# Performance work log

Measured on AMD Instinct MI355X. Metric: run time of the kernel, lower is better.

## Reference

```python
import jax, jax.numpy as jnp
import numpy as np

C = 256

def setup_inputs() -> dict:
    key = jax.random.key(0)
    ks = jax.random.split(key, 8)
    B, H, W = 4, 64, 64
    x = jax.random.normal(ks[0], (B, C, H, W), dtype=jnp.float32)
    # 1x1 conv weights ~ kaiming uniform; bias zero
    bound = np.sqrt(6.0 / C)
    Wq = jax.random.uniform(ks[1], (C, C), minval=-bound, maxval=bound, dtype=jnp.float32)
    Wk = jax.random.uniform(ks[2], (C, C), minval=-bound, maxval=bound, dtype=jnp.float32)
    Wv = jax.random.uniform(ks[3], (C, C), minval=-bound, maxval=bound, dtype=jnp.float32)
    bq = jnp.zeros((C,), jnp.float32)
    bk = jnp.zeros((C,), jnp.float32)
    bv = jnp.zeros((C,), jnp.float32)
    # gamma initialized to zero in torch; use small nonzero so output depends on attn path
    gamma = jnp.array([0.1], dtype=jnp.float32)
    return {"x": x, "Wq": Wq, "bq": bq, "Wk": Wk, "bk": bk, "Wv": Wv, "bv": bv, "gamma": gamma}


def reference(x, Wq, bq, Wk, bk, Wv, bv, gamma):
    B, Cc, H, W = x.shape
    N = H * W
    xf = x.reshape(B, Cc, N)  # [B,C,N]
    # 1x1 conv == per-pixel linear over channels: out[b,o,n] = sum_c W[o,c]*x[b,c,n] + b[o]
    q = jnp.einsum('oc,bcn->bon', Wq, xf) + bq[None, :, None]  # [B,C,N]
    k = jnp.einsum('oc,bcn->bon', Wk, xf) + bk[None, :, None]
    v = jnp.einsum('oc,bcn->bon', Wv, xf) + bv[None, :, None]
    # energy[b,i,j] = q[b,:,i] . k[b,:,j]  (no scaling, as in source)
    energy = jnp.einsum('bci,bcj->bij', q, k)  # [B,N,N]
    attention = jax.nn.softmax(energy, axis=-1)
    # out[b,c,i] = sum_j v[b,c,j] * attention[b,i,j]  (bmm(value, attn^T))
    out = jnp.einsum('bcj,bij->bci', v, attention)
    out = out.reshape(B, Cc, H, W)
    return gamma * out + x
```

## Files before the change

kernel.cpp:

```cpp
#include <hip/hip_runtime.h>
#include <hip/hip_bf16.h>
#include <cstdint>


#define C_DIM 256
#define N_DIM 4096
#define B_DIM 4

typedef _Float16 f16;
typedef f16 f16x8 __attribute__((ext_vector_type(8)));
typedef f16 f16x4 __attribute__((ext_vector_type(4)));
typedef float f32x4 __attribute__((ext_vector_type(4)));

__device__ __forceinline__ void dma16(const f16* g, f16* l) {
  __builtin_amdgcn_global_load_lds(
      (const __attribute__((address_space(1))) unsigned int*)g,
      (__attribute__((address_space(3))) unsigned int*)l, 16, 0, 0);
}

__global__ __launch_bounds__(256) void k_prep_xs(const float* __restrict__ x,
                                                 f16* __restrict__ xs) {
  __shared__ float tile[64][65];
  const int b = blockIdx.z, nb = blockIdx.x * 64, cb = blockIdx.y * 64;
  const float* xb = x + (size_t)b * C_DIM * N_DIM;
  for (int i = threadIdx.x; i < 64 * 64; i += 256) {
    int c = i >> 6, n = i & 63;
    tile[c][n] = xb[(size_t)(cb + c) * N_DIM + nb + n];
  }
  __syncthreads();
  f16* xsb = xs + (size_t)b * N_DIM * C_DIM;
  for (int i = threadIdx.x; i < 64 * 64; i += 256) {
    int n = i >> 6, c = i & 63;
    xsb[(size_t)(nb + n) * C_DIM + cb + c] = (f16)tile[c][n];
  }
}

__global__ __launch_bounds__(256) void k_cast_w(const float* __restrict__ Wq,
                                                const float* __restrict__ Wk,
                                                const float* __restrict__ Wv,
                                                f16* __restrict__ Wh) {
  int i = blockIdx.x * 256 + threadIdx.x;
  int sel = i >> 16, j = i & 65535;
  const float* s = (sel == 0) ? Wq : (sel == 1) ? Wk : Wv;
  Wh[i] = (f16)s[j];
}

__global__ __launch_bounds__(256) void k_proj(const f16* __restrict__ xs,
                                              const f16* __restrict__ Wh,
                                              const float* __restrict__ bq,
                                              const float* __restrict__ bk,
                                              const float* __restrict__ bv,
                                              f16* __restrict__ Qh,
                                              f16* __restrict__ Kh,
                                              f16* __restrict__ Vh) {
  const int z = blockIdx.y;
  const int w = threadIdx.x >> 6, lane = threadIdx.x & 63;
  const int quad = lane >> 4, li = lane & 15;
  const f16* W = Wh + (size_t)z * 65536;
  const float* bias = (z == 0) ? bq : (z == 1) ? bk : bv;

  if (z < 2) {
    f16* out = (z == 0) ? Qh : Kh;
    const int g0 = (blockIdx.x * 4 + w) * 16;
    f16x8 a[8];
    const f16* arow = xs + (size_t)(g0 + li) * C_DIM + quad * 8;
#pragma unroll
    for (int kf = 0; kf < 8; kf++) a[kf] = *(const f16x8*)(arow + kf * 32);
    for (int ot = 0; ot < 16; ot++) {
      f32x4 acc = {0.f, 0.f, 0.f, 0.f};
      const f16* brow = W + (size_t)(ot * 16 + li) * C_DIM + quad * 8;
#pragma unroll
      for (int kf = 0; kf < 8; kf++) {
        f16x8 bf = *(const f16x8*)(brow + kf * 32);
        acc = __builtin_amdgcn_mfma_f32_16x16x32_f16(a[kf], bf, acc, 0, 0, 0);
      }
      float bb = bias[ot * 16 + li];
      f16* orow = out + (size_t)g0 * C_DIM + ot * 16 + li;
#pragma unroll
      for (int r = 0; r < 4; r++)
        orow[(size_t)(quad * 4 + r) * C_DIM] = (f16)(acc[r] + bb);
    }
  } else {
    const int t = blockIdx.x * 4 + w;
    const int b = t >> 8, j0 = (t & 255) * 16;
    f16x8 bfr[8];
    const f16* brow = xs + (size_t)(b * N_DIM + j0 + li) * C_DIM + quad * 8;
#pragma unroll
    for (int kf = 0; kf < 8; kf++) bfr[kf] = *(const f16x8*)(brow + kf * 32);
    for (int ot = 0; ot < 16; ot++) {
      f32x4 acc = {0.f, 0.f, 0.f, 0.f};
      const f16* arow = W + (size_t)(ot * 16 + li) * C_DIM + quad * 8;
#pragma unroll
      for (int kf = 0; kf < 8; kf++) {
        f16x8 af = *(const f16x8*)(arow + kf * 32);
        acc = __builtin_amdgcn_mfma_f32_16x16x32_f16(af, bfr[kf], acc, 0, 0, 0);
      }
      f16* obase = Vh + ((size_t)(b * C_DIM + ot * 16 + quad * 4)) * N_DIM + j0 + li;
#pragma unroll
      for (int r = 0; r < 4; r++) {
        float bb = bias[ot * 16 + quad * 4 + r];
        obase[(size_t)r * N_DIM] = (f16)(acc[r] + bb);
      }
    }
  }
}

#define JT 64
#define NT (N_DIM / JT)
#define K0_OFF 0
#define K1_OFF 16384
#define V0_OFF 32768
#define V1_OFF 49152
#define P_OFF  65536
#define PSTR 72
#define SMEM_F16 70144

__global__ __launch_bounds__(256, 1) void k_attn(const f16* __restrict__ Qh,
                                                 const f16* __restrict__ Kh,
                                                 const f16* __restrict__ Vh,
                                                 const float* __restrict__ x,
                                                 const float* __restrict__ gamma_p,
                                                 float* __restrict__ out) {
  __shared__ __align__(16) f16 smem[SMEM_F16];
  const int b = blockIdx.y;
  const int tid = threadIdx.x;
  const int w = tid >> 6, lane = tid & 63;
  const int quad = lane >> 4, li = lane & 15;
  const int lw = li & 7;
  const int ibase = blockIdx.x * 64 + w * 16;

  int ksl[8];
#pragma unroll
  for (int kf = 0; kf < 8; kf++) ksl[kf] = ((kf * 4 + quad) ^ lw) << 3;
  const int vsl0 = (quad ^ lw) << 3;

  f16x8 qf[8];
  {
    const f16* qrow = Qh + (size_t)(b * N_DIM + ibase + li) * C_DIM + quad * 8;
#pragma unroll
    for (int kf = 0; kf < 8; kf++) qf[kf] = *(const f16x8*)(qrow + kf * 32);
  }
  const f16* Kb = Kh + (size_t)b * N_DIM * C_DIM;
  const f16* Vb = Vh + (size_t)b * C_DIM * N_DIM;
  f16* Pw = smem + P_OFF + w * 16 * PSTR;

  const float LOG2E = 1.4426950408889634f;
  float m = -3.0e38f, l = 0.0f;
  f32x4 acc[16];
#pragma unroll
  for (int ct = 0; ct < 16; ct++) acc[ct] = (f32x4){0.f, 0.f, 0.f, 0.f};

  {
    const f16* kg = Kb;
    const f16* vg = Vb;
#pragma unroll
    for (int it = 0; it < 8; it++) {
      int p = w * 8 + it;
      int krsw = (2 * it + (lane >> 5)) & 7;
      dma16(kg + (size_t)(2 * p + (lane >> 5)) * C_DIM + (((lane & 31) ^ krsw) * 8),
            smem + K0_OFF + p * 512);
      dma16(vg + (size_t)(p * 8 + (lane >> 3)) * N_DIM + (((lane & 7) ^ (lane >> 3)) * 8),
            smem + V0_OFF + p * 512);
    }
  }
  __syncthreads();

  for (int t = 0; t < NT; t++) {
    const f16* Kc = smem + ((t & 1) ? K1_OFF : K0_OFF);
    const f16* Vc = smem + ((t & 1) ? V1_OFF : V0_OFF);

    if (t + 1 < NT) {
      f16* Kn = smem + ((t & 1) ? K0_OFF : K1_OFF);
      f16* Vn = smem + ((t & 1) ? V0_OFF : V1_OFF);
      const int jt = (t + 1) * JT;
      const f16* kg = Kb + (size_t)jt * C_DIM;
      const f16* vg = Vb + jt;
#pragma unroll
      for (int it = 0; it < 8; it++) {
        int p = w * 8 + it;
        int krsw = (2 * it + (lane >> 5)) & 7;
        dma16(kg + (size_t)(2 * p + (lane >> 5)) * C_DIM + (((lane & 31) ^ krsw) * 8),
              Kn + p * 512);
        dma16(vg + (size_t)(p * 8 + (lane >> 3)) * N_DIM + (((lane & 7) ^ (lane >> 3)) * 8),
              Vn + p * 512);
      }
    }

    f32x4 s[4];
#pragma unroll
    for (int sub = 0; sub < 4; sub++) {
      f32x4 ss = {0.f, 0.f, 0.f, 0.f};
      const f16* krow = Kc + (sub * 16 + li) * 256;
#pragma unroll
      for (int kf = 0; kf < 8; kf++) {
        f16x8 kfr = *(const f16x8*)(krow + ksl[kf]);
        ss = __builtin_amdgcn_mfma_f32_16x16x32_f16(kfr, qf[kf], ss, 0, 0, 0);
      }
      s[sub] = ss;
    }

    float tm = -3.0e38f;
#pragma unroll
    for (int sub = 0; sub < 4; sub++)
      tm = fmaxf(tm, fmaxf(fmaxf(s[sub][0], s[sub][1]), fmaxf(s[sub][2], s[sub][3])));
    tm = fmaxf(tm, __shfl_xor(tm, 16));
    tm = fmaxf(tm, __shfl_xor(tm, 32));
    float nm = fmaxf(m, tm);
    float alpha = exp2f((m - nm) * LOG2E);
    m = nm;
    if (__any(alpha < 1.0f)) {
      l *= alpha;
#pragma unroll
      for (int ct = 0; ct < 16; ct++) {
        acc[ct][0] *= alpha; acc[ct][1] *= alpha;
        acc[ct][2] *= alpha; acc[ct][3] *= alpha;
      }
    }
#pragma unroll
    for (int sub = 0; sub < 4; sub++) {
      float p0 = exp2f((s[sub][0] - m) * LOG2E);
      float p1 = exp2f((s[sub][1] - m) * LOG2E);
      float p2 = exp2f((s[sub][2] - m) * LOG2E);
      float p3 = exp2f((s[sub][3] - m) * LOG2E);
      l += (p0 + p1) + (p2 + p3);
      *(f16x4*)(Pw + li * PSTR + sub * 16 + quad * 4) =
          (f16x4){(f16)p0, (f16)p1, (f16)p2, (f16)p3};
    }

    f16x8 pf0 = *(const f16x8*)(Pw + li * PSTR + quad * 8);
    f16x8 pf1 = *(const f16x8*)(Pw + li * PSTR + 32 + quad * 8);
#pragma unroll
    for (int ct = 0; ct < 16; ct++) {
      const f16* vrow = Vc + (ct * 16 + li) * 64;
      f16x8 v0 = *(const f16x8*)(vrow + vsl0);
      f16x8 v1 = *(const f16x8*)(vrow + (vsl0 ^ 32));
      acc[ct] = __builtin_amdgcn_mfma_f32_16x16x32_f16(v0, pf0, acc[ct], 0, 0, 0);
      acc[ct] = __builtin_amdgcn_mfma_f32_16x16x32_f16(v1, pf1, acc[ct], 0, 0, 0);
    }

    __syncthreads();
  }

  l += __shfl_xor(l, 16);
  l += __shfl_xor(l, 32);
  const float scale = gamma_p[0] / l;

  const float* xb = x + (size_t)b * C_DIM * N_DIM;
  float* ob = out + (size_t)b * C_DIM * N_DIM;
  const int icol = ibase + li;
#pragma unroll
  for (int ct = 0; ct < 16; ct++) {
#pragma unroll
    for (int r = 0; r < 4; r++) {
      size_t off = (size_t)(ct * 16 + quad * 4 + r) * N_DIM + icol;
      ob[off] = acc[ct][r] * scale + xb[off];
    }
  }
}

extern "C" void kernel_launch(void* const* d_in, const int* in_sizes, int n_in,
                              void* d_out, int out_size, void* d_ws, size_t ws_size,
                              hipStream_t stream) {
  const float* x     = (const float*)d_in[0];
  const float* Wq    = (const float*)d_in[1];
  const float* bq    = (const float*)d_in[2];
  const float* Wk    = (const float*)d_in[3];
  const float* bk    = (const float*)d_in[4];
  const float* Wv    = (const float*)d_in[5];
  const float* bv    = (const float*)d_in[6];
  const float* gamma = (const float*)d_in[7];
  float* out = (float*)d_out;

  char* ws = (char*)d_ws;
  f16* xs = (f16*)(ws);
  f16* Qh = (f16*)(ws + (size_t)8  * 1024 * 1024);
  f16* Kh = (f16*)(ws + (size_t)16 * 1024 * 1024);
  f16* Vh = (f16*)(ws + (size_t)24 * 1024 * 1024);
  f16* Wh = (f16*)(ws + (size_t)32 * 1024 * 1024);

  k_prep_xs<<<dim3(64, 4, 4), 256, 0, stream>>>(x, xs);
  k_cast_w<<<dim3(768), 256, 0, stream>>>(Wq, Wk, Wv, Wh);
  k_proj<<<dim3(256, 3), 256, 0, stream>>>(xs, Wh, bq, bk, bv, Qh, Kh, Vh);
  k_attn<<<dim3(64, 4), 256, 0, stream>>>(Qh, Kh, Vh, x, gamma, out);
}
```

Measured before the change: 294.6 us.

## Split each key tile across two wave groups with flash-style merge

The attention kernel doubles to 512 threads (8 waves). Each group of four waves processes half of every 64-key tile, keeping its own running max, sum and accumulators. At the end, the two halves are combined through shared memory with a log-sum-exp rescale. This is meant to double resident waves per CU, since there is only one block per CU, and so hide more MFMA and LDS latency. The cost is a cross-wave merge, extra shared-memory traffic, and twice as many waves holding large accumulator register sets.

Result: faster. 258.6 us (-12.2%).

```diff
diff --git a/kernel.cpp b/kernel.cpp
--- a/kernel.cpp
+++ b/kernel.cpp
@@ -112,10 +112,13 @@
 #define V0_OFF 32768
 #define V1_OFF 49152
 #define P_OFF  65536
-#define PSTR 72
-#define SMEM_F16 70144
-
-__global__ __launch_bounds__(256, 1) void k_attn(const f16* __restrict__ Qh,
+#define PSTR 40
+#define SMEM_F16 70656
+#define MRG_WSTR 4160
+#define MRG_CSTR 260
+#define ML_OFF   16640
+
+__global__ __launch_bounds__(512, 1) void k_attn(const f16* __restrict__ Qh,
                                                  const f16* __restrict__ Kh,
                                                  const f16* __restrict__ Vh,
                                                  const float* __restrict__ x,
@@ -125,14 +128,15 @@
   const int b = blockIdx.y;
   const int tid = threadIdx.x;
   const int w = tid >> 6, lane = tid & 63;
+  const int wq = w & 3, wj = w >> 2;
   const int quad = lane >> 4, li = lane & 15;
   const int lw = li & 7;
-  const int ibase = blockIdx.x * 64 + w * 16;
+  const int ibase = blockIdx.x * 64 + wq * 16;
 
   int ksl[8];
 #pragma unroll
   for (int kf = 0; kf < 8; kf++) ksl[kf] = ((kf * 4 + quad) ^ lw) << 3;
-  const int vsl0 = (quad ^ lw) << 3;
+  const int vsl = ((wj * 4 + quad) ^ lw) << 3;
 
   f16x8 qf[8];
   {
@@ -151,15 +155,13 @@
   for (int ct = 0; ct < 16; ct++) acc[ct] = (f32x4){0.f, 0.f, 0.f, 0.f};
 
   {
-    const f16* kg = Kb;
-    const f16* vg = Vb;
-#pragma unroll
-    for (int it = 0; it < 8; it++) {
-      int p = w * 8 + it;
+#pragma unroll
+    for (int it = 0; it < 4; it++) {
+      int p = w * 4 + it;
       int krsw = (2 * it + (lane >> 5)) & 7;
-      dma16(kg + (size_t)(2 * p + (lane >> 5)) * C_DIM + (((lane & 31) ^ krsw) * 8),
+      dma16(Kb + (size_t)(2 * p + (lane >> 5)) * C_DIM + (((lane & 31) ^ krsw) * 8),
             smem + K0_OFF + p * 512);
-      dma16(vg + (size_t)(p * 8 + (lane >> 3)) * N_DIM + (((lane & 7) ^ (lane >> 3)) * 8),
+      dma16(Vb + (size_t)(p * 8 + (lane >> 3)) * N_DIM + (((lane & 7) ^ (lane >> 3)) * 8),
             smem + V0_OFF + p * 512);
     }
   }
@@ -176,8 +178,8 @@
       const f16* kg = Kb + (size_t)jt * C_DIM;
       const f16* vg = Vb + jt;
 #pragma unroll
-      for (int it = 0; it < 8; it++) {
-        int p = w * 8 + it;
+      for (int it = 0; it < 4; it++) {
+        int p = w * 4 + it;
         int krsw = (2 * it + (lane >> 5)) & 7;
         dma16(kg + (size_t)(2 * p + (lane >> 5)) * C_DIM + (((lane & 31) ^ krsw) * 8),
               Kn + p * 512);
@@ -186,11 +188,11 @@
       }
     }
 
-    f32x4 s[4];
-#pragma unroll
-    for (int sub = 0; sub < 4; sub++) {
+    f32x4 s[2];
+#pragma unroll
+    for (int sub = 0; sub < 2; sub++) {
       f32x4 ss = {0.f, 0.f, 0.f, 0.f};
-      const f16* krow = Kc + (sub * 16 + li) * 256;
+      const f16* krow = Kc + (wj * 32 + sub * 16 + li) * 256;
 #pragma unroll
       for (int kf = 0; kf < 8; kf++) {
         f16x8 kfr = *(const f16x8*)(krow + ksl[kf]);
@@ -199,10 +201,8 @@
       s[sub] = ss;
     }
 
-    float tm = -3.0e38f;
-#pragma unroll
-    for (int sub = 0; sub < 4; sub++)
-      tm = fmaxf(tm, fmaxf(fmaxf(s[sub][0], s[sub][1]), fmaxf(s[sub][2], s[sub][3])));
+    float tm = fmaxf(fmaxf(fmaxf(s[0][0], s[0][1]), fmaxf(s[0][2], s[0][3])),
+                     fmaxf(fmaxf(s[1][0], s[1][1]), fmaxf(s[1][2], s[1][3])));
     tm = fmaxf(tm, __shfl_xor(tm, 16));
     tm = fmaxf(tm, __shfl_xor(tm, 32));
     float nm = fmaxf(m, tm);
@@ -217,7 +217,7 @@
       }
     }
 #pragma unroll
-    for (int sub = 0; sub < 4; sub++) {
+    for (int sub = 0; sub < 2; sub++) {
       float p0 = exp2f((s[sub][0] - m) * LOG2E);
       float p1 = exp2f((s[sub][1] - m) * LOG2E);
       float p2 = exp2f((s[sub][2] - m) * LOG2E);
@@ -227,15 +227,12 @@
           (f16x4){(f16)p0, (f16)p1, (f16)p2, (f16)p3};
     }
 
-    f16x8 pf0 = *(const f16x8*)(Pw + li * PSTR + quad * 8);
-    f16x8 pf1 = *(const f16x8*)(Pw + li * PSTR + 32 + quad * 8);
+    f16x8 pf = *(const f16x8*)(Pw + li * PSTR + quad * 8);
 #pragma unroll
     for (int ct = 0; ct < 16; ct++) {
       const f16* vrow = Vc + (ct * 16 + li) * 64;
-      f16x8 v0 = *(const f16x8*)(vrow + vsl0);
-      f16x8 v1 = *(const f16x8*)(vrow + (vsl0 ^ 32));
-      acc[ct] = __builtin_amdgcn_mfma_f32_16x16x32_f16(v0, pf0, acc[ct], 0, 0, 0);
-      acc[ct] = __builtin_amdgcn_mfma_f32_16x16x32_f16(v1, pf1, acc[ct], 0, 0, 0);
+      f16x8 v = *(const f16x8*)(vrow + vsl);
+      acc[ct] = __builtin_amdgcn_mfma_f32_16x16x32_f16(v, pf, acc[ct], 0, 0, 0);
     }
 
     __syncthreads();
@@ -243,17 +240,42 @@
 
   l += __shfl_xor(l, 16);
   l += __shfl_xor(l, 32);
-  const float scale = gamma_p[0] / l;
-
-  const float* xb = x + (size_t)b * C_DIM * N_DIM;
-  float* ob = out + (size_t)b * C_DIM * N_DIM;
-  const int icol = ibase + li;
-#pragma unroll
-  for (int ct = 0; ct < 16; ct++) {
-#pragma unroll
-    for (int r = 0; r < 4; r++) {
-      size_t off = (size_t)(ct * 16 + quad * 4 + r) * N_DIM + icol;
-      ob[off] = acc[ct][r] * scale + xb[off];
+
+  float* mrg = (float*)smem;
+  if (wj == 1) {
+    const int u = wq;
+    float* base = mrg + u * MRG_WSTR + li * MRG_CSTR;
+#pragma unroll
+    for (int ct = 0; ct < 16; ct++)
+      *(f32x4*)(base + ct * 16 + quad * 4) = acc[ct];
+    if (lane < 16) {
+      mrg[ML_OFF + u * 32 + li] = m;
+      mrg[ML_OFF + u * 32 + 16 + li] = l;
+    }
+  }
+  __syncthreads();
+  if (wj == 0) {
+    const int u = wq;
+    const float m_b = mrg[ML_OFF + u * 32 + li];
+    const float l_b = mrg[ML_OFF + u * 32 + 16 + li];
+    const float M = fmaxf(m, m_b);
+    const float aa = exp2f((m - M) * LOG2E);
+    const float ab = exp2f((m_b - M) * LOG2E);
+    const float lm = aa * l + ab * l_b;
+    const float scale = gamma_p[0] / lm;
+    const float* base = mrg + u * MRG_WSTR + li * MRG_CSTR;
+
+    const float* xb = x + (size_t)b * C_DIM * N_DIM;
+    float* ob = out + (size_t)b * C_DIM * N_DIM;
+    const int icol = ibase + li;
+#pragma unroll
+    for (int ct = 0; ct < 16; ct++) {
+      f32x4 accb = *(const f32x4*)(base + ct * 16 + quad * 4);
+#pragma unroll
+      for (int r = 0; r < 4; r++) {
+        size_t off = (size_t)(ct * 16 + quad * 4 + r) * N_DIM + icol;
+        ob[off] = (acc[ct][r] * aa + accb[r] * ab) * scale + xb[off];
+      }
     }
   }
 }
@@ -281,5 +303,5 @@
   k_prep_xs<<<dim3(64, 4, 4), 256, 0, stream>>>(x, xs);
   k_cast_w<<<dim3(768), 256, 0, stream>>>(Wq, Wk, Wv, Wh);
   k_proj<<<dim3(256, 3), 256, 0, stream>>>(xs, Wh, bq, bk, bv, Qh, Kh, Vh);
-  k_attn<<<dim3(64, 4), 256, 0, stream>>>(Qh, Kh, Vh, x, gamma, out);
-}
+  k_attn<<<dim3(64, 4), 512, 0, stream>>>(Qh, Kh, Vh, x, gamma, out);
+}
```
